# Kernel tuning notes

Hardware: AMD Instinct MI355X
Metric: run time of the kernel (lower is better)

The kernel has to match this reference:

```python
import jax, jax.numpy as jnp
import numpy as np

N, K, F_IN, F_HID, F_OUT = 500000, 16, 7, 40, 3

def setup_inputs() -> dict:
    key = jax.random.key(0)
    k1, k2, k3 = jax.random.split(key, 3)
    mailbox = jax.random.normal(k1, (N, K, F_IN), dtype=jnp.float32)
    W1 = jax.random.normal(k2, (F_IN, F_HID), dtype=jnp.float32) * (1.0 / np.sqrt(F_IN))
    b1 = jnp.zeros((F_HID,), dtype=jnp.float32)
    W2 = jax.random.normal(k3, (F_HID, F_OUT), dtype=jnp.float32) * (1.0 / np.sqrt(F_HID))
    b2 = jnp.zeros((F_OUT,), dtype=jnp.float32)
    return {"mailbox": mailbox, "W1": W1, "b1": b1, "W2": W2, "b2": b2}

def reference(mailbox, W1, b1, W2, b2):
    # MLP 7->40->3 applied per (node, neighbor) message, then mean over neighbors.
    h = jax.nn.relu(jnp.einsum('nkf,fh->nkh', mailbox, W1) + b1)  # [N,K,40]
    y = jnp.einsum('nkh,ho->nko', h, W2) + b2                     # [N,K,3]
    return jnp.mean(y, axis=1)                                    # [N,3]
```

## Files before the change

### kernel.cpp

```cpp
#include <hip/hip_runtime.h>
#include <stdint.h>

#define N_NODES 500000
#define K_NB 16
#define F_IN 7
#define F_HID 40
#define F_OUT 3
#define NODE_FLOATS (K_NB * F_IN)
#define NPW 16
#define WPB 4
#define NPB (NPW * WPB)
#define NBLK ((N_NODES + NPB - 1) / NPB)

typedef float v2f __attribute__((ext_vector_type(2)));

typedef __attribute__((address_space(3))) void lds_void_t;
typedef __attribute__((address_space(1))) const void glb_void_t;
typedef __attribute__((address_space(4))) const float kfloat;

__global__ void prep_kernel(const float* __restrict__ W1,
                            const float* __restrict__ b1,
                            const float* __restrict__ W2,
                            float* __restrict__ ws)
{
    const int t = threadIdx.x;
    if (t < F_HID) {
        float* p = ws + t * 8;
        #pragma unroll
        for (int i = 0; i < F_IN; ++i) p[i] = W1[i * F_HID + t];
        p[7] = b1[t];
    } else if (t < 2 * F_HID) {
        const int h = t - F_HID;
        float* p = ws + F_HID * 8 + h * 4;
        p[0] = W2[h * F_OUT + 0];
        p[1] = W2[h * F_OUT + 1];
        p[2] = W2[h * F_OUT + 2];
        p[3] = 0.0f;
    }
}

__global__ __launch_bounds__(256) void aggre_kernel(
    const float* __restrict__ mailbox,
    const float* __restrict__ wtab,
    const float* __restrict__ w2tab,
    const float* __restrict__ b2,
    float* __restrict__ out)
{
    __shared__ __align__(16) float tile[WPB][NPW * NODE_FLOATS];

    const int t = threadIdx.x;
    const int wave = t >> 6;
    const int lane = t & 63;
    const long tile0 = (long)blockIdx.x * NPB + (long)wave * NPW;
    if (tile0 >= N_NODES) return;

    const float* gsrc = mailbox + (size_t)tile0 * NODE_FLOATS;
    #pragma unroll
    for (int j = 0; j < 7; ++j) {
        const float* g = gsrc + (size_t)(j * 64 + lane) * 4;
        __builtin_amdgcn_global_load_lds(
            (glb_void_t*)g,
            (lds_void_t*)&tile[wave][j * 256],
            16, 0, 0);
    }
    __builtin_amdgcn_s_waitcnt(0x0f70);

    const int nloc = lane >> 2;
    const int r = lane & 3;
    const int base = nloc * NODE_FLOATS + r * 28;
    v2f mA[F_IN], mB[F_IN];
    #pragma unroll
    for (int j = 0; j < F_IN; ++j) {
        v2f a, b;
        a.x = tile[wave][base + j];
        a.y = tile[wave][base + 7 + j];
        b.x = tile[wave][base + 14 + j];
        b.y = tile[wave][base + 21 + j];
        mA[j] = a;
        mB[j] = b;
    }

    const kfloat* wt  = (const kfloat*)(uintptr_t)wtab;
    const kfloat* w2t = (const kfloat*)(uintptr_t)w2tab;

    const v2f zero = {0.0f, 0.0f};
    v2f a0 = zero, a1 = zero, a2 = zero;

    #pragma unroll 4
    for (int h = 0; h < F_HID; ++h) {
        const float w0 = wt[h * 8 + 0];
        const float w1 = wt[h * 8 + 1];
        const float w2 = wt[h * 8 + 2];
        const float w3 = wt[h * 8 + 3];
        const float w4 = wt[h * 8 + 4];
        const float w5 = wt[h * 8 + 5];
        const float w6 = wt[h * 8 + 6];
        const float bb = wt[h * 8 + 7];

        const v2f wv0 = {w0, w0}, wv1 = {w1, w1}, wv2 = {w2, w2};
        const v2f wv3 = {w3, w3}, wv4 = {w4, w4}, wv5 = {w5, w5};
        const v2f wv6 = {w6, w6}, bbv = {bb, bb};

        v2f accA = mA[0] * wv0;
        v2f accB = mB[0] * wv0;
        accA = __builtin_elementwise_fma(mA[1], wv1, accA);
        accB = __builtin_elementwise_fma(mB[1], wv1, accB);
        accA = __builtin_elementwise_fma(mA[2], wv2, accA);
        accB = __builtin_elementwise_fma(mB[2], wv2, accB);
        accA = __builtin_elementwise_fma(mA[3], wv3, accA);
        accB = __builtin_elementwise_fma(mB[3], wv3, accB);
        accA = __builtin_elementwise_fma(mA[4], wv4, accA);
        accB = __builtin_elementwise_fma(mB[4], wv4, accB);
        accA = __builtin_elementwise_fma(mA[5], wv5, accA);
        accB = __builtin_elementwise_fma(mB[5], wv5, accB);
        accA = __builtin_elementwise_fma(mA[6], wv6, accA);
        accB = __builtin_elementwise_fma(mB[6], wv6, accB);

        accA = __builtin_elementwise_max(accA + bbv, zero);
        accB = __builtin_elementwise_max(accB + bbv, zero);
        const v2f sh = accA + accB;

        const float u0 = w2t[h * 4 + 0];
        const float u1 = w2t[h * 4 + 1];
        const float u2 = w2t[h * 4 + 2];
        const v2f uv0 = {u0, u0}, uv1 = {u1, u1}, uv2 = {u2, u2};
        a0 = __builtin_elementwise_fma(sh, uv0, a0);
        a1 = __builtin_elementwise_fma(sh, uv1, a1);
        a2 = __builtin_elementwise_fma(sh, uv2, a2);
    }

    float s0 = a0.x + a0.y;
    float s1 = a1.x + a1.y;
    float s2 = a2.x + a2.y;
    s0 += __shfl_xor(s0, 1); s0 += __shfl_xor(s0, 2);
    s1 += __shfl_xor(s1, 1); s1 += __shfl_xor(s1, 2);
    s2 += __shfl_xor(s2, 1); s2 += __shfl_xor(s2, 2);

    if (r < F_OUT) {
        const float val = (r == 0) ? s0 : ((r == 1) ? s1 : s2);
        out[(size_t)(tile0 + nloc) * F_OUT + r] =
            fmaf(val, 1.0f / (float)K_NB, b2[r]);
    }
}

extern "C" void kernel_launch(void* const* d_in, const int* in_sizes, int n_in,
                              void* d_out, int out_size, void* d_ws, size_t ws_size,
                              hipStream_t stream) {
    const float* mailbox = (const float*)d_in[0];
    const float* W1      = (const float*)d_in[1];
    const float* b1      = (const float*)d_in[2];
    const float* W2      = (const float*)d_in[3];
    const float* b2      = (const float*)d_in[4];
    float* ws  = (float*)d_ws;
    float* out = (float*)d_out;

    prep_kernel<<<1, 128, 0, stream>>>(W1, b1, W2, ws);

    const float* wtab  = ws;
    const float* w2tab = ws + F_HID * 8;
    aggre_kernel<<<NBLK, 256, 0, stream>>>(mailbox, wtab, w2tab, b2, out);
}
```

Measured before the change: 317.9 us.

## Make aggregation kernel persistent with double-buffered LDS prefetch per wave

Replaces the one-tile-per-wave grid with a fixed grid of 512 blocks whose waves loop over tiles with a grid stride. Each wave prefetches the next 16-node tile into a second LDS buffer with async global-to-LDS loads while computing the current tile, using vmcnt waits to overlap memory with compute. This trades launch and wave-scheduling overhead for lower resident parallelism and doubled LDS per block. Unused b2 register loads remain.

```diff
diff --git a/kernel.cpp b/kernel.cpp
--- a/kernel.cpp
+++ b/kernel.cpp
@@ -9,8 +9,10 @@
 #define NODE_FLOATS (K_NB * F_IN)
 #define NPW 16
 #define WPB 4
-#define NPB (NPW * WPB)
-#define NBLK ((N_NODES + NPB - 1) / NPB)
+#define TILE_FLOATS (NPW * NODE_FLOATS)
+#define NT (N_NODES / NPW)
+#define GRID_BLOCKS 512
+#define NW (GRID_BLOCKS * WPB)
 
 typedef float v2f __attribute__((ext_vector_type(2)));
 
@@ -46,101 +48,121 @@
     const float* __restrict__ b2,
     float* __restrict__ out)
 {
-    __shared__ __align__(16) float tile[WPB][NPW * NODE_FLOATS];
+    __shared__ __align__(16) float tile[WPB][2][TILE_FLOATS];
 
-    const int t = threadIdx.x;
+    const int t  = threadIdx.x;
     const int wave = t >> 6;
     const int lane = t & 63;
-    const long tile0 = (long)blockIdx.x * NPB + (long)wave * NPW;
-    if (tile0 >= N_NODES) return;
+    const int wid = blockIdx.x * WPB + wave;
 
-    const float* gsrc = mailbox + (size_t)tile0 * NODE_FLOATS;
-    #pragma unroll
-    for (int j = 0; j < 7; ++j) {
-        const float* g = gsrc + (size_t)(j * 64 + lane) * 4;
-        __builtin_amdgcn_global_load_lds(
-            (glb_void_t*)g,
-            (lds_void_t*)&tile[wave][j * 256],
-            16, 0, 0);
-    }
-    __builtin_amdgcn_s_waitcnt(0x0f70);
+    const kfloat* wt  = (const kfloat*)(uintptr_t)wtab;
+    const kfloat* w2t = (const kfloat*)(uintptr_t)w2tab;
+    const float bo0 = b2[0], bo1 = b2[1], bo2 = b2[2];
 
     const int nloc = lane >> 2;
     const int r = lane & 3;
-    const int base = nloc * NODE_FLOATS + r * 28;
-    v2f mA[F_IN], mB[F_IN];
-    #pragma unroll
-    for (int j = 0; j < F_IN; ++j) {
-        v2f a, b;
-        a.x = tile[wave][base + j];
-        a.y = tile[wave][base + 7 + j];
-        b.x = tile[wave][base + 14 + j];
-        b.y = tile[wave][base + 21 + j];
-        mA[j] = a;
-        mB[j] = b;
+    const int mbase = nloc * NODE_FLOATS + r * 28;
+
+    long tt = wid;
+    {
+        const float* g0 = mailbox + (size_t)tt * TILE_FLOATS;
+        #pragma unroll
+        for (int j = 0; j < 7; ++j) {
+            __builtin_amdgcn_global_load_lds(
+                (glb_void_t*)(g0 + (size_t)(j * 64 + lane) * 4),
+                (lds_void_t*)&tile[wave][0][j * 256], 16, 0, 0);
+        }
     }
+    int parity = 0;
 
-    const kfloat* wt  = (const kfloat*)(uintptr_t)wtab;
-    const kfloat* w2t = (const kfloat*)(uintptr_t)w2tab;
+    while (true) {
+        const long tn = tt + NW;
+        if (tn < NT) {
+            __builtin_amdgcn_s_waitcnt(0xC07F);
+            const float* g = mailbox + (size_t)tn * TILE_FLOATS;
+            #pragma unroll
+            for (int j = 0; j < 7; ++j) {
+                __builtin_amdgcn_global_load_lds(
+                    (glb_void_t*)(g + (size_t)(j * 64 + lane) * 4),
+                    (lds_void_t*)&tile[wave][parity ^ 1][j * 256], 16, 0, 0);
+            }
+            __builtin_amdgcn_s_waitcnt(0x0F77);
+        } else {
+            __builtin_amdgcn_s_waitcnt(0x0F70);
+        }
 
-    const v2f zero = {0.0f, 0.0f};
-    v2f a0 = zero, a1 = zero, a2 = zero;
+        const float* tb = &tile[wave][parity][0];
+        v2f mA[F_IN], mB[F_IN];
+        #pragma unroll
+        for (int j = 0; j < F_IN; ++j) {
+            v2f a, b;
+            a.x = tb[mbase + j];
+            a.y = tb[mbase + 7 + j];
+            b.x = tb[mbase + 14 + j];
+            b.y = tb[mbase + 21 + j];
+            mA[j] = a;
+            mB[j] = b;
+        }
 
-    #pragma unroll 4
-    for (int h = 0; h < F_HID; ++h) {
-        const float w0 = wt[h * 8 + 0];
-        const float w1 = wt[h * 8 + 1];
-        const float w2 = wt[h * 8 + 2];
-        const float w3 = wt[h * 8 + 3];
-        const float w4 = wt[h * 8 + 4];
-        const float w5 = wt[h * 8 + 5];
-        const float w6 = wt[h * 8 + 6];
-        const float bb = wt[h * 8 + 7];
+        const v2f zero = {0.0f, 0.0f};
+        v2f a0 = zero, a1 = zero, a2 = zero;
 
-        const v2f wv0 = {w0, w0}, wv1 = {w1, w1}, wv2 = {w2, w2};
-        const v2f wv3 = {w3, w3}, wv4 = {w4, w4}, wv5 = {w5, w5};
-        const v2f wv6 = {w6, w6}, bbv = {bb, bb};
+        #pragma unroll 4
+        for (int h = 0; h < F_HID; ++h) {
+            const float w0 = wt[h * 8 + 0], w1 = wt[h * 8 + 1];
+            const float w2 = wt[h * 8 + 2], w3 = wt[h * 8 + 3];
+            const float w4 = wt[h * 8 + 4], w5 = wt[h * 8 + 5];
+            const float w6 = wt[h * 8 + 6], bb = wt[h * 8 + 7];
+            const v2f wv0 = {w0, w0}, wv1 = {w1, w1}, wv2 = {w2, w2};
+            const v2f wv3 = {w3, w3}, wv4 = {w4, w4}, wv5 = {w5, w5};
+            const v2f wv6 = {w6, w6}, bbv = {bb, bb};
 
-        v2f accA = mA[0] * wv0;
-        v2f accB = mB[0] * wv0;
-        accA = __builtin_elementwise_fma(mA[1], wv1, accA);
-        accB = __builtin_elementwise_fma(mB[1], wv1, accB);
-        accA = __builtin_elementwise_fma(mA[2], wv2, accA);
-        accB = __builtin_elementwise_fma(mB[2], wv2, accB);
-        accA = __builtin_elementwise_fma(mA[3], wv3, accA);
-        accB = __builtin_elementwise_fma(mB[3], wv3, accB);
-        accA = __builtin_elementwise_fma(mA[4], wv4, accA);
-        accB = __builtin_elementwise_fma(mB[4], wv4, accB);
-        accA = __builtin_elementwise_fma(mA[5], wv5, accA);
-        accB = __builtin_elementwise_fma(mB[5], wv5, accB);
-        accA = __builtin_elementwise_fma(mA[6], wv6, accA);
-        accB = __builtin_elementwise_fma(mB[6], wv6, accB);
+            v2f accA = mA[0] * wv0;
+            v2f accB = mB[0] * wv0;
+            accA = __builtin_elementwise_fma(mA[1], wv1, accA);
+            accB = __builtin_elementwise_fma(mB[1], wv1, accB);
+            accA = __builtin_elementwise_fma(mA[2], wv2, accA);
+            accB = __builtin_elementwise_fma(mB[2], wv2, accB);
+            accA = __builtin_elementwise_fma(mA[3], wv3, accA);
+            accB = __builtin_elementwise_fma(mB[3], wv3, accB);
+            accA = __builtin_elementwise_fma(mA[4], wv4, accA);
+            accB = __builtin_elementwise_fma(mB[4], wv4, accB);
+            accA = __builtin_elementwise_fma(mA[5], wv5, accA);
+            accB = __builtin_elementwise_fma(mB[5], wv5, accB);
+            accA = __builtin_elementwise_fma(mA[6], wv6, accA);
+            accB = __builtin_elementwise_fma(mB[6], wv6, accB);
 
-        accA = __builtin_elementwise_max(accA + bbv, zero);
-        accB = __builtin_elementwise_max(accB + bbv, zero);
-        const v2f sh = accA + accB;
+            accA = __builtin_elementwise_max(accA + bbv, zero);
+            accB = __builtin_elementwise_max(accB + bbv, zero);
+            const v2f sh = accA + accB;
 
-        const float u0 = w2t[h * 4 + 0];
-        const float u1 = w2t[h * 4 + 1];
-        const float u2 = w2t[h * 4 + 2];
-        const v2f uv0 = {u0, u0}, uv1 = {u1, u1}, uv2 = {u2, u2};
-        a0 = __builtin_elementwise_fma(sh, uv0, a0);
-        a1 = __builtin_elementwise_fma(sh, uv1, a1);
-        a2 = __builtin_elementwise_fma(sh, uv2, a2);
+            const float u0 = w2t[h * 4 + 0];
+            const float u1 = w2t[h * 4 + 1];
+            const float u2 = w2t[h * 4 + 2];
+            const v2f uv0 = {u0, u0}, uv1 = {u1, u1}, uv2 = {u2, u2};
+            a0 = __builtin_elementwise_fma(sh, uv0, a0);
+            a1 = __builtin_elementwise_fma(sh, uv1, a1);
+            a2 = __builtin_elementwise_fma(sh, uv2, a2);
+        }
+
+        float s0 = a0.x + a0.y;
+        float s1 = a1.x + a1.y;
+        float s2 = a2.x + a2.y;
+        s0 += __shfl_xor(s0, 1); s0 += __shfl_xor(s0, 2);
+        s1 += __shfl_xor(s1, 1); s1 += __shfl_xor(s1, 2);
+        s2 += __shfl_xor(s2, 1); s2 += __shfl_xor(s2, 2);
+
+        if (r < F_OUT) {
+            const float val = (r == 0) ? s0 : ((r == 1) ? s1 : s2);
+            out[((size_t)tt * NPW + nloc) * F_OUT + r] =
+                fmaf(val, 1.0f / (float)K_NB, b2[r]);
+        }
+
+        if (tn >= NT) break;
+        tt = tn;
+        parity ^= 1;
     }
-
-    float s0 = a0.x + a0.y;
-    float s1 = a1.x + a1.y;
-    float s2 = a2.x + a2.y;
-    s0 += __shfl_xor(s0, 1); s0 += __shfl_xor(s0, 2);
-    s1 += __shfl_xor(s1, 1); s1 += __shfl_xor(s1, 2);
-    s2 += __shfl_xor(s2, 1); s2 += __shfl_xor(s2, 2);
-
-    if (r < F_OUT) {
-        const float val = (r == 0) ? s0 : ((r == 1) ? s1 : s2);
-        out[(size_t)(tile0 + nloc) * F_OUT + r] =
-            fmaf(val, 1.0f / (float)K_NB, b2[r]);
-    }
+    (void)bo0; (void)bo1; (void)bo2;
 }
 
 extern "C" void kernel_launch(void* const* d_in, const int* in_sizes, int n_in,
@@ -158,5 +180,5 @@
 
     const float* wtab  = ws;
     const float* w2tab = ws + F_HID * 8;
-    aggre_kernel<<<NBLK, 256, 0, stream>>>(mailbox, wtab, w2tab, b2, out);
+    aggre_kernel<<<GRID_BLOCKS, 256, 0, stream>>>(mailbox, wtab, w2tab, b2, out);
 }
```

After: 322.5 us. No clear change (+1.4%).
